# Kernel optimization log

Hardware: AMD Instinct MI355X
Metric: run time of the kernel (lower is better)

## Reference

```python
import jax, jax.numpy as jnp
import numpy as np

B, T, C, H = 8, 2048, 1024, 64


def build_rope_cache(seq_len, dim):
    half = dim // 2
    inv_freq = 1.0 / (10000.0 ** (jnp.arange(half, dtype=jnp.float32) / half))
    t = jnp.arange(seq_len, dtype=jnp.float32)
    freqs = t[:, None] * inv_freq[None, :]          # (T, half)
    cos = jnp.repeat(jnp.cos(freqs), 2, axis=-1)    # (T, dim) interleaved
    sin = jnp.repeat(jnp.sin(freqs), 2, axis=-1)
    return cos, sin


def apply_rope(x, cos, sin):
    # x: (B, T, H); cos/sin: (T, H)
    x1 = x[..., ::2]
    x2 = x[..., 1::2]
    rot = jnp.stack([-x2, x1], axis=-1).reshape(x.shape)
    return x * cos[None] + rot * sin[None]


def setup_inputs() -> dict:
    key = jax.random.key(0)
    kx, kq, kk, kv = jax.random.split(key, 4)
    scale = 1.0 / np.sqrt(C)
    return {
        "x": jax.random.normal(kx, (B, T, C), dtype=jnp.float32),
        "Wq": jax.random.normal(kq, (C, H), dtype=jnp.float32) * scale,
        "Wk": jax.random.normal(kk, (C, H), dtype=jnp.float32) * scale,
        "Wv": jax.random.normal(kv, (C, H), dtype=jnp.float32) * scale,
    }


def reference(x, Wq, Wk, Wv):
    Bc, Tc, _ = x.shape
    head_size = Wq.shape[1]
    cos, sin = build_rope_cache(Tc, head_size)

    q = apply_rope(x @ Wq, cos, sin)   # (B, T, H)
    k = apply_rope(x @ Wk, cos, sin)   # (B, T, H)
    v = x @ Wv                          # (B, T, H)

    # full TxT masked softmax attention (matches original non-fused path)
    wei = jnp.einsum('bth,bsh->bts', q, k) * (head_size ** -0.5)  # (B, T, T)
    causal = jnp.tril(jnp.ones((Tc, Tc), dtype=bool))
    wei = jnp.where(causal[None], wei, -jnp.inf)
    wei = jax.nn.softmax(wei, axis=-1)
    # dropout p=0 (eval mode) -> identity
    return jnp.einsum('bts,bsh->bth', wei, v)
```

## Files before the change

### kernel.cpp

```cpp
#include <hip/hip_runtime.h>
#include <cmath>

#define Tn  2048
#define Cn  1024
#define Hn  64
#define BTn 16384

typedef _Float16 f16x8 __attribute__((ext_vector_type(8)));
typedef _Float16 f16x4 __attribute__((ext_vector_type(4)));
typedef _Float16 f16x2 __attribute__((ext_vector_type(2)));
typedef float    f32x4 __attribute__((ext_vector_type(4)));

#define MFMA16(a, b, c) __builtin_amdgcn_mfma_f32_16x16x32_f16(a, b, c, 0, 0, 0)

__global__ __launch_bounds__(256) void prep_w_kernel(
    const float* __restrict__ Wq, const float* __restrict__ Wk,
    const float* __restrict__ Wv, _Float16* __restrict__ Wt)
{
    __shared__ float ts[64][65];
    const int blk = blockIdx.x;
    const int p   = blk >> 4;
    const int c0  = (blk & 15) * 64;
    const float* __restrict__ W = (p == 0) ? Wq : (p == 1) ? Wk : Wv;
    const int tid = threadIdx.x;
    #pragma unroll
    for (int it = 0; it < 16; it++) {
        int idx = tid + it * 256;
        int c = idx >> 6, n = idx & 63;
        ts[c][n] = W[(size_t)(c0 + c) * Hn + n];
    }
    __syncthreads();
    #pragma unroll
    for (int it = 0; it < 16; it++) {
        int idx = tid + it * 256;
        int n = idx >> 6, c = idx & 63;
        Wt[(size_t)(p * 64 + n) * Cn + c0 + c] = (_Float16)ts[c][n];
    }
}

__global__ __launch_bounds__(512) void proj_kernel(
    const float* __restrict__ x, const _Float16* __restrict__ Wt,
    _Float16* __restrict__ qh, _Float16* __restrict__ kh_out, _Float16* __restrict__ vT)
{
    __shared__ __align__(16) f32x4 pbuf[6 * 256];
    const int row0 = blockIdx.x * 32;
    const int tid  = threadIdx.x;
    const int wave = tid >> 6, lane = tid & 63;
    const int kh   = wave >> 2;
    const int wc   = wave & 3;
    const int quad = lane >> 4, l15 = lane & 15;

    f32x4 acc[2][3] = {};
    const _Float16* __restrict__ wb = Wt + (size_t)(wc * 48 + l15) * Cn
                                         + kh * 512 + quad * 8;
    const float* __restrict__ xr0 = x + (size_t)(row0 +      l15) * Cn
                                      + kh * 512 + quad * 8;
    const float* __restrict__ xr1 = x + (size_t)(row0 + 16 + l15) * Cn
                                      + kh * 512 + quad * 8;

    #pragma unroll
    for (int kc = 0; kc < 16; kc++) {
        const int kf = kc * 32;
        f16x8 b0 = *(const f16x8*)&wb[kf];
        f16x8 b1 = *(const f16x8*)&wb[16 * Cn + kf];
        f16x8 b2 = *(const f16x8*)&wb[32 * Cn + kf];
        f32x4 l0 = *(const f32x4*)&xr0[kf];
        f32x4 h0 = *(const f32x4*)&xr0[kf + 4];
        f32x4 l1 = *(const f32x4*)&xr1[kf];
        f32x4 h1 = *(const f32x4*)&xr1[kf + 4];
        f16x8 a0, a1;
        a0[0] = (_Float16)l0[0]; a0[1] = (_Float16)l0[1];
        a0[2] = (_Float16)l0[2]; a0[3] = (_Float16)l0[3];
        a0[4] = (_Float16)h0[0]; a0[5] = (_Float16)h0[1];
        a0[6] = (_Float16)h0[2]; a0[7] = (_Float16)h0[3];
        a1[0] = (_Float16)l1[0]; a1[1] = (_Float16)l1[1];
        a1[2] = (_Float16)l1[2]; a1[3] = (_Float16)l1[3];
        a1[4] = (_Float16)h1[0]; a1[5] = (_Float16)h1[1];
        a1[6] = (_Float16)h1[2]; a1[7] = (_Float16)h1[3];
        acc[0][0] = MFMA16(a0, b0, acc[0][0]);
        acc[1][0] = MFMA16(a1, b0, acc[1][0]);
        acc[0][1] = MFMA16(a0, b1, acc[0][1]);
        acc[1][1] = MFMA16(a1, b1, acc[1][1]);
        acc[0][2] = MFMA16(a0, b2, acc[0][2]);
        acc[1][2] = MFMA16(a1, b2, acc[1][2]);
    }

    if (kh) {
        #pragma unroll
        for (int mt = 0; mt < 2; mt++)
            #pragma unroll
            for (int nt = 0; nt < 3; nt++)
                pbuf[(mt * 3 + nt) * 256 + wc * 64 + lane] = acc[mt][nt];
    }
    __syncthreads();
    if (kh) return;
    #pragma unroll
    for (int mt = 0; mt < 2; mt++)
        #pragma unroll
        for (int nt = 0; nt < 3; nt++)
            acc[mt][nt] += pbuf[(mt * 3 + nt) * 256 + wc * 64 + lane];

    const int bidx = row0 >> 11;
    #pragma unroll
    for (int nt = 0; nt < 3; nt++) {
        const int n = wc * 48 + nt * 16 + l15;
        const int p = n >> 6;
        const int h = n & 63;
        if (p < 2) {
            _Float16* __restrict__ outb = (p == 0) ? qh : kh_out;
            const float invf = __expf(-0.2878231366242557f * (float)(h >> 1));
            #pragma unroll
            for (int mt = 0; mt < 2; mt++) {
                #pragma unroll
                for (int r = 0; r < 4; r++) {
                    int   row = row0 + mt * 16 + quad * 4 + r;
                    float val = acc[mt][nt][r];
                    float partner = __shfl_xor(val, 1, 64);
                    float ang = (float)(row & (Tn - 1)) * invf;
                    float sv, cv;
                    __sincosf(ang, &sv, &cv);
                    float res = (h & 1) ? fmaf(val, cv,  partner * sv)
                                        : fmaf(val, cv, -partner * sv);
                    if (p == 0) res *= 0.125f;
                    float resn = __shfl_xor(res, 1, 64);
                    if (!(l15 & 1)) {
                        f16x2 pk = { (_Float16)res, (_Float16)resn };
                        *(f16x2*)&outb[(size_t)row * Hn + h] = pk;
                    }
                }
            }
        } else {
            #pragma unroll
            for (int mt = 0; mt < 2; mt++) {
                int t = (row0 & (Tn - 1)) + mt * 16 + quad * 4;
                f16x4 pv = { (_Float16)acc[mt][nt][0], (_Float16)acc[mt][nt][1],
                             (_Float16)acc[mt][nt][2], (_Float16)acc[mt][nt][3] };
                *(f16x4*)&vT[((size_t)bidx * Hn + h) * Tn + t] = pv;
            }
        }
    }
}

#define PSP 72

__global__ __launch_bounds__(256, 4) void attn_kernel(
    const _Float16* __restrict__ qh, const _Float16* __restrict__ kh,
    const _Float16* __restrict__ vT, float* __restrict__ out)
{
    __shared__ _Float16 ps[4][16 * PSP];
    __shared__ float ocomb[4][16][65];
    __shared__ float mlcomb[4][2][16];

    const int blk = blockIdx.x;
    const int b   = blk & 7;
    const int j   = blk >> 3;
    const int jm  = j & 31, g = j >> 5;
    const int qt  = (g == 0) ? (127 - jm)
                  : (g == 1) ? (64 + jm)
                  : (g == 2) ? (63 - jm) : jm;
    const int t0  = qt * 16;
    const int tid = threadIdx.x;
    const int w = tid >> 6, lane = tid & 63;
    const int quad = lane >> 4, l15 = lane & 15;

    const _Float16* __restrict__ qb = qh + (size_t)b * Tn * Hn;
    const _Float16* __restrict__ kb = kh + (size_t)b * Tn * Hn;
    const _Float16* __restrict__ vb = vT + (size_t)b * Hn * Tn;

    const f16x8 aq0 = *(const f16x8*)&qb[(size_t)(t0 + l15) * Hn +      quad * 8];
    const f16x8 aq1 = *(const f16x8*)&qb[(size_t)(t0 + l15) * Hn + 32 + quad * 8];

    float m_run[4], l_run[4];
    f32x4 oacc[4] = {};
    #pragma unroll
    for (int r = 0; r < 4; r++) { m_run[r] = -1e30f; l_run[r] = 0.0f; }

    const int nst = (t0 + 16 + 63) >> 6;
    for (int jt = w; jt < nst; jt += 4) {
        const int s0 = jt * 64;

        f16x8 kf[4][2];
        #pragma unroll
        for (int nt = 0; nt < 4; nt++) {
            const _Float16* kp = &kb[(size_t)(s0 + nt * 16 + l15) * Hn + quad * 8];
            kf[nt][0] = *(const f16x8*)kp;
            kf[nt][1] = *(const f16x8*)(kp + 32);
        }
        f32x4 sacc[4];
        #pragma unroll
        for (int nt = 0; nt < 4; nt++) {
            f32x4 z = {};
            z = MFMA16(aq0, kf[nt][0], z);
            z = MFMA16(aq1, kf[nt][1], z);
            sacc[nt] = z;
        }

        f16x8 vf[2][4];
        #pragma unroll
        for (int sc = 0; sc < 2; sc++)
            #pragma unroll
            for (int ht = 0; ht < 4; ht++)
                vf[sc][ht] = *(const f16x8*)&vb[(size_t)(ht * 16 + l15) * Tn
                                                + s0 + sc * 32 + quad * 8];

        if (jt == nst - 1) {
            #pragma unroll
            for (int nt = 0; nt < 4; nt++)
                #pragma unroll
                for (int r = 0; r < 4; r++) {
                    int scol = s0 + nt * 16 + l15;
                    int trow = t0 + quad * 4 + r;
                    if (scol > trow) sacc[nt][r] = -1e30f;
                }
        }

        float pr[4][4];
        #pragma unroll
        for (int r = 0; r < 4; r++) {
            float mx = fmaxf(fmaxf(sacc[0][r], sacc[1][r]),
                             fmaxf(sacc[2][r], sacc[3][r]));
            #pragma unroll
            for (int off = 1; off < 16; off <<= 1)
                mx = fmaxf(mx, __shfl_xor(mx, off, 64));
            float mnew  = fmaxf(m_run[r], mx);
            float alpha = __expf(m_run[r] - mnew);
            m_run[r] = mnew;
            float rs = 0.0f;
            #pragma unroll
            for (int nt = 0; nt < 4; nt++) {
                float pv = __expf(sacc[nt][r] - mnew);
                pr[nt][r] = pv; rs += pv;
            }
            #pragma unroll
            for (int off = 1; off < 16; off <<= 1)
                rs += __shfl_xor(rs, off, 64);
            l_run[r] = fmaf(l_run[r], alpha, rs);
            #pragma unroll
            for (int ht = 0; ht < 4; ht++)
                oacc[ht][r] = oacc[ht][r] * alpha;
        }

        #pragma unroll
        for (int nt = 0; nt < 4; nt++)
            #pragma unroll
            for (int r = 0; r < 4; r++) {
                float pv = pr[nt][r];
                float pn = __shfl_xor(pv, 1, 64);
                if (!(l15 & 1)) {
                    f16x2 pk = { (_Float16)pv, (_Float16)pn };
                    *(f16x2*)&ps[w][(quad * 4 + r) * PSP + nt * 16 + l15] = pk;
                }
            }

        #pragma unroll
        for (int sc = 0; sc < 2; sc++) {
            f16x8 ap = *(const f16x8*)&ps[w][l15 * PSP + sc * 32 + quad * 8];
            #pragma unroll
            for (int ht = 0; ht < 4; ht++)
                oacc[ht] = MFMA16(ap, vf[sc][ht], oacc[ht]);
        }
    }

    #pragma unroll
    for (int r = 0; r < 4; r++) {
        #pragma unroll
        for (int ht = 0; ht < 4; ht++)
            ocomb[w][quad * 4 + r][ht * 16 + l15] = oacc[ht][r];
        if (l15 == 0) {
            mlcomb[w][0][quad * 4 + r] = m_run[r];
            mlcomb[w][1][quad * 4 + r] = l_run[r];
        }
    }
    __syncthreads();

    #pragma unroll
    for (int rp = 0; rp < 4; rp++) {
        int row = w * 4 + rp;
        float m0 = mlcomb[0][0][row], m1 = mlcomb[1][0][row];
        float m2 = mlcomb[2][0][row], m3 = mlcomb[3][0][row];
        float mm = fmaxf(fmaxf(m0, m1), fmaxf(m2, m3));
        float a0 = __expf(m0 - mm), a1 = __expf(m1 - mm);
        float a2 = __expf(m2 - mm), a3 = __expf(m3 - mm);
        float ll = mlcomb[0][1][row] * a0 + mlcomb[1][1][row] * a1
                 + mlcomb[2][1][row] * a2 + mlcomb[3][1][row] * a3;
        float ov = (ocomb[0][row][lane] * a0 + ocomb[1][row][lane] * a1
                  + ocomb[2][row][lane] * a2 + ocomb[3][row][lane] * a3) / ll;
        out[((size_t)b * Tn + t0 + row) * Hn + lane] = ov;
    }
}

extern "C" void kernel_launch(void* const* d_in, const int* in_sizes, int n_in,
                              void* d_out, int out_size, void* d_ws, size_t ws_size,
                              hipStream_t stream) {
    const float* x  = (const float*)d_in[0];
    const float* Wq = (const float*)d_in[1];
    const float* Wk = (const float*)d_in[2];
    const float* Wv = (const float*)d_in[3];

    const size_t qkvN = (size_t)BTn * Hn;
    _Float16* qh = (_Float16*)d_ws;
    _Float16* kh = qh + qkvN;
    _Float16* vT = kh + qkvN;
    _Float16* Wt = vT + qkvN;

    prep_w_kernel<<<48, 256, 0, stream>>>(Wq, Wk, Wv, Wt);
    proj_kernel<<<BTn / 32, 512, 0, stream>>>(x, Wt, qh, kh, vT);
    attn_kernel<<<1024, 256, 0, stream>>>(qh, kh, vT, (float*)d_out);
}
```

Measured before the change: 178.4 us.

## Stage x tile as fp16 in LDS and double rows per projection block

```diff
diff --git a/kernel.cpp b/kernel.cpp
--- a/kernel.cpp
+++ b/kernel.cpp
@@ -38,45 +38,55 @@
     }
 }
 
-__global__ __launch_bounds__(512) void proj_kernel(
+#define XSP 1032
+
+__global__ __launch_bounds__(1024) void proj_kernel(
     const float* __restrict__ x, const _Float16* __restrict__ Wt,
     _Float16* __restrict__ qh, _Float16* __restrict__ kh_out, _Float16* __restrict__ vT)
 {
-    __shared__ __align__(16) f32x4 pbuf[6 * 256];
-    const int row0 = blockIdx.x * 32;
+    extern __shared__ __align__(16) char smem[];
+    _Float16* xs = (_Float16*)smem;
+    const int blk  = blockIdx.x;
     const int tid  = threadIdx.x;
     const int wave = tid >> 6, lane = tid & 63;
-    const int kh   = wave >> 2;
+    const int kh   = wave >> 3;
+    const int mh   = (wave >> 2) & 1;
     const int wc   = wave & 3;
     const int quad = lane >> 4, l15 = lane & 15;
+    const int row0 = blk * 64 + mh * 32;
+
+    {
+        float4 xv[16];
+        #pragma unroll
+        for (int it = 0; it < 16; it++) {
+            int idx = tid + it * 1024;
+            int r = idx >> 8, c4 = idx & 255;
+            xv[it] = *(const float4*)&x[(size_t)(blk * 64 + r) * Cn + c4 * 4];
+        }
+        #pragma unroll
+        for (int it = 0; it < 16; it++) {
+            int idx = tid + it * 1024;
+            int r = idx >> 8, c4 = idx & 255;
+            f16x4 hv = { (_Float16)xv[it].x, (_Float16)xv[it].y,
+                         (_Float16)xv[it].z, (_Float16)xv[it].w };
+            *(f16x4*)&xs[r * XSP + c4 * 4] = hv;
+        }
+    }
+    __syncthreads();
 
     f32x4 acc[2][3] = {};
     const _Float16* __restrict__ wb = Wt + (size_t)(wc * 48 + l15) * Cn
                                          + kh * 512 + quad * 8;
-    const float* __restrict__ xr0 = x + (size_t)(row0 +      l15) * Cn
-                                      + kh * 512 + quad * 8;
-    const float* __restrict__ xr1 = x + (size_t)(row0 + 16 + l15) * Cn
-                                      + kh * 512 + quad * 8;
-
-    #pragma unroll
+    const _Float16* __restrict__ xp = &xs[(mh * 32) * XSP + kh * 512 + quad * 8];
+
+    #pragma unroll 4
     for (int kc = 0; kc < 16; kc++) {
         const int kf = kc * 32;
         f16x8 b0 = *(const f16x8*)&wb[kf];
         f16x8 b1 = *(const f16x8*)&wb[16 * Cn + kf];
         f16x8 b2 = *(const f16x8*)&wb[32 * Cn + kf];
-        f32x4 l0 = *(const f32x4*)&xr0[kf];
-        f32x4 h0 = *(const f32x4*)&xr0[kf + 4];
-        f32x4 l1 = *(const f32x4*)&xr1[kf];
-        f32x4 h1 = *(const f32x4*)&xr1[kf + 4];
-        f16x8 a0, a1;
-        a0[0] = (_Float16)l0[0]; a0[1] = (_Float16)l0[1];
-        a0[2] = (_Float16)l0[2]; a0[3] = (_Float16)l0[3];
-        a0[4] = (_Float16)h0[0]; a0[5] = (_Float16)h0[1];
-        a0[6] = (_Float16)h0[2]; a0[7] = (_Float16)h0[3];
-        a1[0] = (_Float16)l1[0]; a1[1] = (_Float16)l1[1];
-        a1[2] = (_Float16)l1[2]; a1[3] = (_Float16)l1[3];
-        a1[4] = (_Float16)h1[0]; a1[5] = (_Float16)h1[1];
-        a1[6] = (_Float16)h1[2]; a1[7] = (_Float16)h1[3];
+        f16x8 a0 = *(const f16x8*)&xp[(     l15) * XSP + kf];
+        f16x8 a1 = *(const f16x8*)&xp[(16 + l15) * XSP + kf];
         acc[0][0] = MFMA16(a0, b0, acc[0][0]);
         acc[1][0] = MFMA16(a1, b0, acc[1][0]);
         acc[0][1] = MFMA16(a0, b1, acc[0][1]);
@@ -85,12 +95,15 @@
         acc[1][2] = MFMA16(a1, b2, acc[1][2]);
     }
 
+    __syncthreads();
+    f32x4* __restrict__ pbuf = (f32x4*)smem;
+    const int gidx = (mh * 4 + wc) * 6;
     if (kh) {
         #pragma unroll
         for (int mt = 0; mt < 2; mt++)
             #pragma unroll
             for (int nt = 0; nt < 3; nt++)
-                pbuf[(mt * 3 + nt) * 256 + wc * 64 + lane] = acc[mt][nt];
+                pbuf[(gidx + mt * 3 + nt) * 64 + lane] = acc[mt][nt];
     }
     __syncthreads();
     if (kh) return;
@@ -98,9 +111,9 @@
     for (int mt = 0; mt < 2; mt++)
         #pragma unroll
         for (int nt = 0; nt < 3; nt++)
-            acc[mt][nt] += pbuf[(mt * 3 + nt) * 256 + wc * 64 + lane];
-
-    const int bidx = row0 >> 11;
+            acc[mt][nt] += pbuf[(gidx + mt * 3 + nt) * 64 + lane];
+
+    const int bidx = (blk * 64) >> 11;
     #pragma unroll
     for (int nt = 0; nt < 3; nt++) {
         const int n = wc * 48 + nt * 16 + l15;
@@ -303,7 +316,15 @@
     _Float16* vT = kh + qkvN;
     _Float16* Wt = vT + qkvN;
 
+    const int ldsBytes = 64 * XSP * 2;
+    static bool attrSet = false;
+    if (!attrSet) {
+        hipFuncSetAttribute((const void*)proj_kernel,
+                            hipFuncAttributeMaxDynamicSharedMemorySize, ldsBytes);
+        attrSet = true;
+    }
+
     prep_w_kernel<<<48, 256, 0, stream>>>(Wq, Wk, Wv, Wt);
-    proj_kernel<<<BTn / 32, 512, 0, stream>>>(x, Wt, qh, kh, vT);
+    proj_kernel<<<BTn / 64, 1024, ldsBytes, stream>>>(x, Wt, qh, kh, vT);
     attn_kernel<<<1024, 256, 0, stream>>>(qh, kh, vT, (float*)d_out);
 }
```

After: 158.8 us. 11.0% less time.
